# Kernel tuning notes

Hardware: AMD Instinct MI355X
Metric: run time of the kernel (lower is better)

Reference implementation:

```python
import jax, jax.numpy as jnp
import numpy as np

B, T, H = 16384, 64, 64
REG = 300
T10_LO, T10_HI = 0.2, 5.0
M0_LO, M0_HI = 0.1, 20.0


def setup_inputs() -> dict:
    key = jax.random.key(0)
    ks = jax.random.split(key, 40)
    std = 1.0 / np.sqrt(H)
    u = lambda k, shape: jax.random.uniform(k, shape, jnp.float32, -std, std)
    inp = {
        "X_fa": jax.random.normal(ks[0], (B, T), jnp.float32),
        "X_last": jax.random.normal(ks[1], (B, T), jnp.float32),
        "X_mean": jax.random.normal(ks[2], (B, T), jnp.float32),
        "X_mask": (jax.random.uniform(ks[3], (B, T)) < 0.7).astype(jnp.float32),
        "X_delta": jax.random.uniform(ks[4], (B, T), jnp.float32, 0.0, 2.0),
        "fa_vals": jax.random.uniform(ks[5], (B, T), jnp.float32, 0.05, 0.6),
        "TR_vals": jax.random.uniform(ks[6], (B, 1), jnp.float32, 0.003, 0.01),
        # GRU-D cell params (torch Linear convention: y = x @ W.T + b)
        "W_gx": u(ks[7], (1, 1)), "b_gx": u(ks[8], (1,)),
        "W_gh": u(ks[9], (H, 1)), "b_gh": u(ks[10], (H,)),
        "W_xc": u(ks[11], (3 * H, 1)), "b_xc": u(ks[12], (3 * H,)),
        "W_hn": u(ks[13], (H, H)),
        "W_hc": u(ks[14], (2 * H, H)),
        "W_mc": u(ks[15], (3 * H, 1)),
        # attention scores
        "W_sT": u(ks[16], (1, H)), "W_sM": u(ks[17], (1, H)),
        # reg_T10 MLP
        "Wt1": u(ks[18], (REG, H)), "bt1": u(ks[19], (REG,)),
        "Wt2": u(ks[20], (REG, REG)), "bt2": u(ks[21], (REG,)),
        "Wt3": u(ks[22], (1, REG)), "bt3": u(ks[23], (1,)),
        # reg_M0 MLP
        "Wm1": u(ks[24], (REG, H)), "bm1": u(ks[25], (REG,)),
        "Wm2": u(ks[26], (REG, REG)), "bm2": u(ks[27], (REG,)),
        "Wm3": u(ks[28], (1, REG)), "bm3": u(ks[29], (1,)),
    }
    return inp


def _forward(X_fa, X_last, X_mean, X_mask, X_delta, fa_vals, TR_vals,
             W_gx, b_gx, W_gh, b_gh, W_xc, b_xc, W_hn, W_hc, W_mc,
             W_sT, W_sM, Wt1, bt1, Wt2, bt2, Wt3, bt3, Wm1, bm1, Wm2, bm2, Wm3, bm3):
    Bv = X_fa.shape[0]
    Hd = W_gh.shape[0]
    tb = lambda a: a.T[:, :, None]  # [B,T] -> [T,B,1]
    xs = (tb(X_fa), tb(X_mask), tb(X_delta), tb(X_last), tb(X_mean))
    h0 = jnp.zeros((Bv, Hd), X_fa.dtype)

    def step(h, x):
        xi, m, d, xl, xm = x  # each [B,1]
        gx = jnp.exp(-jax.nn.relu(d @ W_gx.T + b_gx))            # [B,1]
        X = m * xi + (1 - m) * gx * xl + (1 - m) * (1 - gx) * xm  # [B,1]
        gh = jnp.exp(-jax.nn.relu(d @ W_gh.T + b_gh))            # [B,H]
        h = gh * h
        x_z, x_r, x_n = jnp.split(X @ W_xc.T + b_xc, 3, axis=1)
        h_z, h_r = jnp.split(h @ W_hc.T, 2, axis=1)
        m_z, m_r, m_n = jnp.split(m @ W_mc.T, 3, axis=1)
        z = jax.nn.sigmoid(x_z + h_z + m_z)
        r = jax.nn.sigmoid(x_r + h_r + m_r)
        h_til = jnp.tanh(x_n + (r * h) @ W_hn.T + m_n)
        h = (1 - z) * h + z * h_til
        return h, (h, X[:, 0])

    _, (out_tbh, Xg_tb) = jax.lax.scan(step, h0, xs)
    out = jnp.transpose(out_tbh, (1, 0, 2))  # [B,T,H]
    X_gru = Xg_tb.T                           # [B,T]

    sT = jax.nn.softmax(out @ W_sT.T, axis=1)  # [B,T,1], softmax over time
    sM = jax.nn.softmax(out @ W_sM.T, axis=1)
    hid_T = jnp.sum(out * sT, axis=1)  # [B,H]
    hid_M = jnp.sum(out * sM, axis=1)

    def reg(h, W1, b1, W2, b2, W3, b3):
        h = jax.nn.elu(h @ W1.T + b1)
        h = jax.nn.elu(h @ W2.T + b2)
        return h @ W3.T + b3  # [B,1]

    t_raw = reg(hid_T, Wt1, bt1, Wt2, bt2, Wt3, bt3)
    m_raw = reg(hid_M, Wm1, bm1, Wm2, bm2, Wm3, bm3)
    T10 = T10_LO + jax.nn.sigmoid(t_raw) * (T10_HI - T10_LO)  # [B,1]
    M0 = M0_LO + jax.nn.sigmoid(m_raw) * (M0_HI - M0_LO)      # [B,1]

    R1 = 1.0 / T10                       # [B,1]
    e = jnp.exp(-TR_vals * R1)           # [B,1]
    X_out = (1 - e) * jnp.sin(fa_vals) / (1 - jnp.cos(fa_vals) * e)  # [B,T]
    X_out = X_out * M0
    return X_out, T10, M0, out, X_gru


def reference(X_fa, X_last, X_mean, X_mask, X_delta, fa_vals, TR_vals,
              W_gx, b_gx, W_gh, b_gh, W_xc, b_xc, W_hn, W_hc, W_mc,
              W_sT, W_sM, Wt1, bt1, Wt2, bt2, Wt3, bt3, Wm1, bm1, Wm2, bm2, Wm3, bm3):
    return _forward(X_fa, X_last, X_mean, X_mask, X_delta, fa_vals, TR_vals,
                    W_gx, b_gx, W_gh, b_gh, W_xc, b_xc, W_hn, W_hc, W_mc,
                    W_sT, W_sM, Wt1, bt1, Wt2, bt2, Wt3, bt3, Wm1, bm1, Wm2, bm2, Wm3, bm3)
```

## Files before the change

### kernel.cpp

```cpp
#include <hip/hip_runtime.h>

#define B_N 16384
#define T_N 64
#define H_N 64
#define XOUT_OFF 0
#define T10_OFF  (B_N * T_N)
#define M0_OFF   (T10_OFF + B_N)
#define OUT_OFF  (M0_OFF + B_N)
#define XGRU_OFF (OUT_OFF + B_N * T_N * H_N)

#define WS_HIDT 0
#define WS_HIDM (WS_HIDT + B_N * 64 * 4)
#define WS_W1T_HI (WS_HIDM + B_N * 64 * 4)
#define WS_W1T_LO (WS_W1T_HI + 304 * 64 * 2)
#define WS_W1M_HI (WS_W1T_LO + 304 * 64 * 2)
#define WS_W1M_LO (WS_W1M_HI + 304 * 64 * 2)
#define WS_W2T_HI (WS_W1M_LO + 304 * 64 * 2)
#define WS_W2T_LO (WS_W2T_HI + 304 * 320 * 2)
#define WS_W2M_HI (WS_W2T_LO + 304 * 320 * 2)
#define WS_W2M_LO (WS_W2M_HI + 304 * 320 * 2)

typedef float  f32x4  __attribute__((ext_vector_type(4)));
typedef __bf16 bf16x8 __attribute__((ext_vector_type(8)));
typedef __bf16 bf16x4 __attribute__((ext_vector_type(4)));

__device__ __forceinline__ f32x4 mfma16(bf16x8 a, bf16x8 b, f32x4 c) {
  return __builtin_amdgcn_mfma_f32_16x16x32_bf16(a, b, c, 0, 0, 0);
}
__device__ __forceinline__ void split8v(const float* v, bf16x8& hi, bf16x8& lo) {
#pragma unroll
  for (int i = 0; i < 8; ++i) {
    __bf16 h = (__bf16)v[i];
    hi[i] = h;
    lo[i] = (__bf16)(v[i] - (float)h);
  }
}
__device__ __forceinline__ void split4v(const float* v, bf16x4& hi, bf16x4& lo) {
#pragma unroll
  for (int i = 0; i < 4; ++i) {
    __bf16 h = (__bf16)v[i];
    hi[i] = h;
    lo[i] = (__bf16)(v[i] - (float)h);
  }
}
__device__ __forceinline__ float sigm(float x) {
  return __builtin_amdgcn_rcpf(1.f + __expf(-x));
}
__device__ __forceinline__ float tanh_f(float x) {
  return 1.f - 2.f * __builtin_amdgcn_rcpf(__expf(2.f * x) + 1.f);
}

__global__ __launch_bounds__(256, 4) void k_gru(
    const float* __restrict__ Xfa, const float* __restrict__ Xlast,
    const float* __restrict__ Xmean, const float* __restrict__ Xmask,
    const float* __restrict__ Xdelta,
    const float* __restrict__ Wgx, const float* __restrict__ bgx,
    const float* __restrict__ Wgh, const float* __restrict__ bgh,
    const float* __restrict__ Wxc, const float* __restrict__ bxc,
    const float* __restrict__ Whn, const float* __restrict__ Whc,
    const float* __restrict__ Wmc,
    const float* __restrict__ WsT, const float* __restrict__ WsM,
    float* __restrict__ dout, float* __restrict__ hidT, float* __restrict__ hidM) {
  __shared__ __align__(16) unsigned char smem[33280];
  const int tid = threadIdx.x;
  const int wv = tid >> 6, l = tid & 63, b16 = l & 15, g4 = l >> 4;
  const int brow = blockIdx.x * 16 + b16;

  for (int c = tid; c < 1536; c += 256) {
    const float* src;
    int row, kc, base;
    if (c < 1024) { row = c >> 3; kc = c & 7; src = Whc + row * 64 + kc * 8; base = 0; }
    else { int c2 = c - 1024; row = c2 >> 3; kc = c2 & 7; src = Whn + row * 64 + kc * 8; base = 16384; }
    float v[8];
    *(float4*)&v[0] = *(const float4*)src;
    *(float4*)&v[4] = *(const float4*)(src + 4);
    bf16x8 hi, lo;
    split8v(v, hi, lo);
    *(bf16x8*)(smem + base + row * 128 + ((kc * 16) ^ ((row & 7) << 4))) = lo;
  }

  const int zrow = wv * 16 + b16;
  const int rrow = 64 + wv * 16 + b16;
  const int nrow = wv * 16 + b16;
  bf16x8 wz_hi[2], wr_hi[2], wn_hi[2];
#pragma unroll
  for (int kt = 0; kt < 2; ++kt) {
    float v[8];
    bf16x8 hi, lo;
    const float* s1 = Whc + zrow * 64 + kt * 32 + g4 * 8;
    *(float4*)&v[0] = *(const float4*)s1; *(float4*)&v[4] = *(const float4*)(s1 + 4);
    split8v(v, hi, lo); wz_hi[kt] = hi;
    const float* s2 = Whc + rrow * 64 + kt * 32 + g4 * 8;
    *(float4*)&v[0] = *(const float4*)s2; *(float4*)&v[4] = *(const float4*)(s2 + 4);
    split8v(v, hi, lo); wr_hi[kt] = hi;
    const float* s3 = Whn + nrow * 64 + kt * 32 + g4 * 8;
    *(float4*)&v[0] = *(const float4*)s3; *(float4*)&v[4] = *(const float4*)(s3 + 4);
    split8v(v, hi, lo); wn_hi[kt] = hi;
  }
  bf16x8 ez = {}, er = {}, en = {};
  if (g4 == 0) {
    const int jz = zrow, jr = rrow, jn = 128 + nrow;
    float Wv, Mv, bv;
    __bf16 wh, mh, bh;
#define MKEXT(dst, WIDX, MIDX, BIDX)                                   \
    Wv = Wxc[WIDX]; Mv = Wmc[MIDX]; bv = bxc[BIDX];                    \
    wh = (__bf16)Wv; mh = (__bf16)Mv; bh = (__bf16)bv;                 \
    dst[0] = wh; dst[1] = (__bf16)(Wv - (float)wh); dst[2] = wh;       \
    dst[3] = mh; dst[4] = (__bf16)(Mv - (float)mh);                    \
    dst[5] = bh; dst[6] = (__bf16)(bv - (float)bh); dst[7] = (__bf16)0.f;
    MKEXT(ez, jz, jz, jz)
    MKEXT(er, jr, jr, jr)
    MKEXT(en, jn, jn, jn)
#undef MKEXT
  }
  float wgh4[4], bgh4[4], wsT4[4], wsM4[4];
#pragma unroll
  for (int i = 0; i < 4; ++i) {
    const int j = wv * 16 + g4 * 4 + i;
    wgh4[i] = Wgh[j]; bgh4[i] = bgh[j];
    wsT4[i] = WsT[j]; wsM4[i] = WsM[j];
  }
  const float wgx0 = Wgx[0], bgx0 = bgx[0];

  __syncthreads();

  float hcur[4] = {}, aT[4] = {}, aM[4] = {};
  float lT = 0.f, lM = 0.f;

  const int ib = brow * T_N;
  float p_xi = Xfa[ib], p_mm = Xmask[ib], p_dd = Xdelta[ib], p_xl = Xlast[ib], p_xm = Xmean[ib];
  const int swz = (b16 & 7) << 4;
  float* outp = dout + OUT_OFF;

  for (int t = 0; t < T_N; ++t) {
    const float xi = p_xi, mm = p_mm, dd = p_dd, xl = p_xl, xm = p_xm;
    const int tn = (t + 1 < T_N) ? t + 1 : T_N - 1;
    p_xi = Xfa[ib + tn]; p_mm = Xmask[ib + tn]; p_dd = Xdelta[ib + tn];
    p_xl = Xlast[ib + tn]; p_xm = Xmean[ib + tn];

    float hd[4];
    {
      float v[4];
#pragma unroll
      for (int i = 0; i < 4; ++i) {
        const float gh = __expf(-fmaxf(0.f, dd * wgh4[i] + bgh4[i]));
        hd[i] = hcur[i] * gh;
        v[i] = hd[i];
      }
      bf16x4 hi4, lo4;
      split4v(v, hi4, lo4);
      const int off = (wv * 32 + g4 * 8) ^ swz;
      *(bf16x4*)(smem + 24576 + b16 * 128 + off) = hi4;
      *(bf16x4*)(smem + 26624 + b16 * 128 + off) = lo4;
    }
    const float gx = __expf(-fmaxf(0.f, dd * wgx0 + bgx0));
    const float X = mm * xi + (1.f - mm) * gx * xl + (1.f - mm) * (1.f - gx) * xm;
    if (wv == 0 && g4 == 0) dout[XGRU_OFF + ib + t] = X;
    bf16x8 bext = {};
    if (g4 == 0) {
      const __bf16 xh = (__bf16)X;
      bext[0] = xh; bext[1] = xh; bext[2] = (__bf16)(X - (float)xh);
      const __bf16 mb = (__bf16)mm;
      bext[3] = mb; bext[4] = mb;
      bext[5] = (__bf16)1.f; bext[6] = (__bf16)1.f; bext[7] = (__bf16)0.f;
    }
    __syncthreads();

    if (t > 0) {
      const f32x4 a = *(const f32x4*)(smem + 32768 + b16 * 32);
      const f32x4 c = *(const f32x4*)(smem + 32768 + b16 * 32 + 16);
      const float pT = __expf(a[0] + a[2] + c[0] + c[2]);
      const float pM = __expf(a[1] + a[3] + c[1] + c[3]);
      lT += pT; lM += pM;
#pragma unroll
      for (int i = 0; i < 4; ++i) { aT[i] += pT * hcur[i]; aM[i] += pM * hcur[i]; }
    }

    f32x4 accZ = {0.f, 0.f, 0.f, 0.f}, accR = {0.f, 0.f, 0.f, 0.f};
#pragma unroll
    for (int kt = 0; kt < 2; ++kt) {
      const int boff = (kt * 64 + g4 * 16) ^ swz;
      const bf16x8 bh = *(const bf16x8*)(smem + 24576 + b16 * 128 + boff);
      const bf16x8 bl = *(const bf16x8*)(smem + 26624 + b16 * 128 + boff);
      const int aoff = (kt * 64 + g4 * 16);
      const bf16x8 zlo = *(const bf16x8*)(smem + zrow * 128 + (aoff ^ ((zrow & 7) << 4)));
      const bf16x8 rlo = *(const bf16x8*)(smem + rrow * 128 + (aoff ^ ((rrow & 7) << 4)));
      accZ = mfma16(wz_hi[kt], bh, accZ);
      accZ = mfma16(zlo, bh, accZ);
      accZ = mfma16(wz_hi[kt], bl, accZ);
      accR = mfma16(wr_hi[kt], bh, accR);
      accR = mfma16(rlo, bh, accR);
      accR = mfma16(wr_hi[kt], bl, accR);
    }
    accZ = mfma16(ez, bext, accZ);
    accR = mfma16(er, bext, accR);

    float zz[4], rh[4];
#pragma unroll
    for (int i = 0; i < 4; ++i) {
      zz[i] = sigm(accZ[i]);
      rh[i] = sigm(accR[i]) * hd[i];
    }
    {
      bf16x4 hi4, lo4;
      split4v(rh, hi4, lo4);
      const int off = (wv * 32 + g4 * 8) ^ swz;
      *(bf16x4*)(smem + 28672 + b16 * 128 + off) = hi4;
      *(bf16x4*)(smem + 30720 + b16 * 128 + off) = lo4;
    }
    __syncthreads();

    f32x4 accN = {0.f, 0.f, 0.f, 0.f};
#pragma unroll
    for (int kt = 0; kt < 2; ++kt) {
      const int boff = (kt * 64 + g4 * 16) ^ swz;
      const bf16x8 ch = *(const bf16x8*)(smem + 28672 + b16 * 128 + boff);
      const bf16x8 cl = *(const bf16x8*)(smem + 30720 + b16 * 128 + boff);
      const bf16x8 nlo =
          *(const bf16x8*)(smem + 16384 + nrow * 128 + ((kt * 64 + g4 * 16) ^ ((nrow & 7) << 4)));
      accN = mfma16(wn_hi[kt], ch, accN);
      accN = mfma16(nlo, ch, accN);
      accN = mfma16(wn_hi[kt], cl, accN);
    }
    accN = mfma16(en, bext, accN);

    f32x4 ho;
    float scT = 0.f, scM = 0.f;
#pragma unroll
    for (int i = 0; i < 4; ++i) {
      const float ht = tanh_f(accN[i]);
      const float hn = (1.f - zz[i]) * hd[i] + zz[i] * ht;
      hcur[i] = hn;
      ho[i] = hn;
      scT += hn * wsT4[i];
      scM += hn * wsM4[i];
    }
    *(f32x4*)(outp + (ib + t) * 64 + wv * 16 + g4 * 4) = ho;
    scT += __shfl_xor(scT, 16); scT += __shfl_xor(scT, 32);
    scM += __shfl_xor(scM, 16); scM += __shfl_xor(scM, 32);
    if (l < 16) {
      float2 sc = {scT, scM};
      *(float2*)(smem + 32768 + b16 * 32 + wv * 8) = sc;
    }
  }
  __syncthreads();
  {
    const f32x4 a = *(const f32x4*)(smem + 32768 + b16 * 32);
    const f32x4 c = *(const f32x4*)(smem + 32768 + b16 * 32 + 16);
    const float pT = __expf(a[0] + a[2] + c[0] + c[2]);
    const float pM = __expf(a[1] + a[3] + c[1] + c[3]);
    lT += pT; lM += pM;
#pragma unroll
    for (int i = 0; i < 4; ++i) { aT[i] += pT * hcur[i]; aM[i] += pM * hcur[i]; }
  }
  const float invT = 1.f / lT, invM = 1.f / lM;
  f32x4 vT, vM;
#pragma unroll
  for (int i = 0; i < 4; ++i) { vT[i] = aT[i] * invT; vM[i] = aM[i] * invM; }
  *(f32x4*)(hidT + brow * 64 + wv * 16 + g4 * 4) = vT;
  *(f32x4*)(hidM + brow * 64 + wv * 16 + g4 * 4) = vM;
}

__device__ __forceinline__ void wsplit(float v, unsigned short* hi, unsigned short* lo, int idx) {
  union { __bf16 b; unsigned short u; } c;
  __bf16 hb = (__bf16)v;
  c.b = hb; hi[idx] = c.u;
  c.b = (__bf16)(v - (float)hb); lo[idx] = c.u;
}
__global__ void k_prep(const float* __restrict__ Wt1, const float* __restrict__ Wm1,
                       const float* __restrict__ Wt2, const float* __restrict__ Wm2,
                       unsigned short* w1t_hi, unsigned short* w1t_lo,
                       unsigned short* w1m_hi, unsigned short* w1m_lo,
                       unsigned short* w2t_hi, unsigned short* w2t_lo,
                       unsigned short* w2m_hi, unsigned short* w2m_lo) {
  const int i = blockIdx.x * 256 + threadIdx.x;
  if (i < 304 * 64) {
    const int r = i >> 6, c = i & 63;
    const float vt = (r < 300) ? Wt1[r * 64 + c] : 0.f;
    const float vm = (r < 300) ? Wm1[r * 64 + c] : 0.f;
    wsplit(vt, w1t_hi, w1t_lo, i);
    wsplit(vm, w1m_hi, w1m_lo, i);
  }
  {
    const int r = i / 320, c = i - r * 320;
    const bool ok = (r < 300) && (c < 300);
    const float vt = ok ? Wt2[r * 300 + c] : 0.f;
    const float vm = ok ? Wm2[r * 300 + c] : 0.f;
    wsplit(vt, w2t_hi, w2t_lo, i);
    wsplit(vm, w2m_hi, w2m_lo, i);
  }
}

__global__ __launch_bounds__(256, 2) void k_mlp(
    const float* __restrict__ hidT, const float* __restrict__ hidM,
    const unsigned short* __restrict__ w1t_hi, const unsigned short* __restrict__ w1t_lo,
    const unsigned short* __restrict__ w1m_hi, const unsigned short* __restrict__ w1m_lo,
    const unsigned short* __restrict__ w2t_hi, const unsigned short* __restrict__ w2t_lo,
    const unsigned short* __restrict__ w2m_hi, const unsigned short* __restrict__ w2m_lo,
    const float* __restrict__ bt1, const float* __restrict__ bt2,
    const float* __restrict__ Wt3, const float* __restrict__ bt3,
    const float* __restrict__ bm1, const float* __restrict__ bm2,
    const float* __restrict__ Wm3, const float* __restrict__ bm3,
    float* __restrict__ dout) {
  __shared__ __align__(16) unsigned char smem[44608];
  const int tid = threadIdx.x;
  const int blk = blockIdx.x & 255;
  const bool isM = blockIdx.x >= 256;
  const float* hid = isM ? hidM : hidT;
  const unsigned short* w1hi = isM ? w1m_hi : w1t_hi;
  const unsigned short* w1lo = isM ? w1m_lo : w1t_lo;
  const unsigned short* w2hi = isM ? w2m_hi : w2t_hi;
  const unsigned short* w2lo = isM ? w2m_lo : w2t_lo;
  const float* b1 = isM ? bm1 : bt1;
  const float* b2 = isM ? bm2 : bt2;
  const float* w3 = isM ? Wm3 : Wt3;
  const float b3 = (isM ? bm3 : bt3)[0];
  const float LOV = isM ? 0.1f : 0.2f;
  const float HIV = isM ? 20.f : 5.0f;
  float* headp = dout + (isM ? M0_OFF : T10_OFF);

  float* sb1 = (float*)(smem + 40960);
  float* sb2 = (float*)(smem + 42176);
  float* sw3 = (float*)(smem + 43392);
  for (int i = tid; i < 304; i += 256) {
    sb1[i] = (i < 300) ? b1[i] : 0.f;
    sb2[i] = (i < 300) ? b2[i] : 0.f;
    sw3[i] = (i < 300) ? w3[i] : 0.f;
  }
  __syncthreads();

  const int wv = tid >> 6, l = tid & 63, b16 = l & 15, g4 = l >> 4;
  const int b = blk * 64 + wv * 16 + b16;
  const int h1off = wv * 10240;

  bf16x8 b1h[2], b1l[2];
#pragma unroll
  for (int kt = 0; kt < 2; ++kt) {
    const float* hp = hid + b * 64 + kt * 32 + g4 * 8;
    float v[8];
    *(float4*)&v[0] = *(const float4*)hp;
    *(float4*)&v[4] = *(const float4*)(hp + 4);
    split8v(v, b1h[kt], b1l[kt]);
  }
  f32x4 acc1[19];
#pragma unroll
  for (int jt = 0; jt < 19; ++jt) {
    f32x4 acc = {0.f, 0.f, 0.f, 0.f};
#pragma unroll
    for (int kt = 0; kt < 2; ++kt) {
      const int row = jt * 16 + b16;
      bf16x8 ahi = *(const bf16x8*)(w1hi + row * 64 + kt * 32 + g4 * 8);
      bf16x8 alo = *(const bf16x8*)(w1lo + row * 64 + kt * 32 + g4 * 8);
      acc = mfma16(ahi, b1h[kt], acc);
      acc = mfma16(alo, b1h[kt], acc);
      acc = mfma16(ahi, b1l[kt], acc);
    }
    acc1[jt] = acc;
  }
  if (g4 == 0) {
#pragma unroll
    for (int q = 0; q < 4; ++q) {
      const int off = (608 + q * 8) ^ ((b16 & 7) << 4);
      *(unsigned long long*)(smem + h1off + b16 * 640 + off) = 0ull;
    }
  }
#pragma unroll
  for (int jt = 0; jt < 19; ++jt) {
    bf16x4 hv;
#pragma unroll
    for (int i = 0; i < 4; ++i) {
      const int j = jt * 16 + g4 * 4 + i;
      const float v = acc1[jt][i] + sb1[j];
      const float e = (v > 0.f) ? v : (__expf(v) - 1.f);
      hv[i] = (__bf16)e;
    }
    const int off = (jt * 32 + g4 * 8) ^ ((b16 & 7) << 4);
    *(bf16x4*)(smem + h1off + b16 * 640 + off) = hv;
  }
  bf16x8 bh2[10];
#pragma unroll
  for (int kt = 0; kt < 10; ++kt) {
    const int off = (kt * 64 + g4 * 16) ^ ((b16 & 7) << 4);
    bh2[kt] = *(const bf16x8*)(smem + h1off + b16 * 640 + off);
  }
  float raw = 0.f;
#pragma unroll
  for (int jt = 0; jt < 19; ++jt) {
    f32x4 acc = {0.f, 0.f, 0.f, 0.f};
#pragma unroll
    for (int kt = 0; kt < 10; ++kt) {
      const int row = jt * 16 + b16;
      bf16x8 ahi = *(const bf16x8*)(w2hi + row * 320 + kt * 32 + g4 * 8);
      bf16x8 alo = *(const bf16x8*)(w2lo + row * 320 + kt * 32 + g4 * 8);
      acc = mfma16(ahi, bh2[kt], acc);
      acc = mfma16(alo, bh2[kt], acc);
    }
#pragma unroll
    for (int i = 0; i < 4; ++i) {
      const int j = jt * 16 + g4 * 4 + i;
      const float v = acc[i] + sb2[j];
      const float e = (v > 0.f) ? v : (__expf(v) - 1.f);
      raw += e * sw3[j];
    }
  }
  raw += __shfl_xor(raw, 16);
  raw += __shfl_xor(raw, 32);
  if (l < 16) {
    const float rr = raw + b3;
    headp[b] = LOV + (HIV - LOV) / (1.f + __expf(-rr));
  }
}

__global__ void k_final(const float* __restrict__ fav, const float* __restrict__ TR,
                        float* __restrict__ dout) {
  const int i = blockIdx.x * 256 + threadIdx.x;
  const int bb = i >> 6;
  const float T10v = dout[T10_OFF + bb];
  const float M0v = dout[M0_OFF + bb];
  const float e = __expf(-TR[bb] / T10v);
  const float fa = fav[i];
  float s, c;
  __sincosf(fa, &s, &c);
  dout[i] = (1.f - e) * s / (1.f - c * e) * M0v;
}

extern "C" void kernel_launch(void* const* d_in, const int* in_sizes, int n_in,
                              void* d_out, int out_size, void* d_ws, size_t ws_size,
                              hipStream_t stream) {
  const float* Xfa   = (const float*)d_in[0];
  const float* Xlast = (const float*)d_in[1];
  const float* Xmean = (const float*)d_in[2];
  const float* Xmask = (const float*)d_in[3];
  const float* Xdelta= (const float*)d_in[4];
  const float* fav   = (const float*)d_in[5];
  const float* TR    = (const float*)d_in[6];
  const float* Wgx   = (const float*)d_in[7];
  const float* bgx   = (const float*)d_in[8];
  const float* Wgh   = (const float*)d_in[9];
  const float* bgh   = (const float*)d_in[10];
  const float* Wxc   = (const float*)d_in[11];
  const float* bxc   = (const float*)d_in[12];
  const float* Whn   = (const float*)d_in[13];
  const float* Whc   = (const float*)d_in[14];
  const float* Wmc   = (const float*)d_in[15];
  const float* WsT   = (const float*)d_in[16];
  const float* WsM   = (const float*)d_in[17];
  const float* Wt1   = (const float*)d_in[18];
  const float* bt1   = (const float*)d_in[19];
  const float* Wt2   = (const float*)d_in[20];
  const float* bt2   = (const float*)d_in[21];
  const float* Wt3   = (const float*)d_in[22];
  const float* bt3   = (const float*)d_in[23];
  const float* Wm1   = (const float*)d_in[24];
  const float* bm1   = (const float*)d_in[25];
  const float* Wm2   = (const float*)d_in[26];
  const float* bm2   = (const float*)d_in[27];
  const float* Wm3   = (const float*)d_in[28];
  const float* bm3   = (const float*)d_in[29];

  float* dout = (float*)d_out;
  char* ws = (char*)d_ws;
  float* hidT = (float*)(ws + WS_HIDT);
  float* hidM = (float*)(ws + WS_HIDM);
  unsigned short* w1t_hi = (unsigned short*)(ws + WS_W1T_HI);
  unsigned short* w1t_lo = (unsigned short*)(ws + WS_W1T_LO);
  unsigned short* w1m_hi = (unsigned short*)(ws + WS_W1M_HI);
  unsigned short* w1m_lo = (unsigned short*)(ws + WS_W1M_LO);
  unsigned short* w2t_hi = (unsigned short*)(ws + WS_W2T_HI);
  unsigned short* w2t_lo = (unsigned short*)(ws + WS_W2T_LO);
  unsigned short* w2m_hi = (unsigned short*)(ws + WS_W2M_HI);
  unsigned short* w2m_lo = (unsigned short*)(ws + WS_W2M_LO);

  k_prep<<<380, 256, 0, stream>>>(Wt1, Wm1, Wt2, Wm2, w1t_hi, w1t_lo, w1m_hi, w1m_lo,
                                  w2t_hi, w2t_lo, w2m_hi, w2m_lo);
  k_gru<<<1024, 256, 0, stream>>>(Xfa, Xlast, Xmean, Xmask, Xdelta, Wgx, bgx, Wgh, bgh, Wxc, bxc,
                                  Whn, Whc, Wmc, WsT, WsM, dout, hidT, hidM);
  k_mlp<<<512, 256, 0, stream>>>(hidT, hidM, w1t_hi, w1t_lo, w1m_hi, w1m_lo, w2t_hi, w2t_lo,
                                 w2m_hi, w2m_lo, bt1, bt2, Wt3, bt3, bm1, bm2, Wm3, bm3, dout);
  k_final<<<4096, 256, 0, stream>>>(fav, TR, dout);
}
```

Before: 697.0 us.

## Stage GRU outputs in LDS for coalesced stores, keep Whn lo in registers

```diff
diff --git a/kernel.cpp b/kernel.cpp
--- a/kernel.cpp
+++ b/kernel.cpp
@@ -49,6 +49,20 @@
 __device__ __forceinline__ float tanh_f(float x) {
   return 1.f - 2.f * __builtin_amdgcn_rcpf(__expf(2.f * x) + 1.f);
 }
+__device__ __forceinline__ void wave_barrier() {
+  asm volatile("s_waitcnt lgkmcnt(0)" ::: "memory");
+  __builtin_amdgcn_s_barrier();
+  __builtin_amdgcn_sched_barrier(0);
+}
+
+#define OS_WHCLO 0
+#define OS_HDH 16384
+#define OS_HDL 18432
+#define OS_RHH 20480
+#define OS_RHL 22528
+#define OS_SC  24576
+#define OS_OST 25088
+#define OS_XST 29440
 
 __global__ __launch_bounds__(256, 4) void k_gru(
     const float* __restrict__ Xfa, const float* __restrict__ Xlast,
@@ -61,28 +75,26 @@
     const float* __restrict__ Wmc,
     const float* __restrict__ WsT, const float* __restrict__ WsM,
     float* __restrict__ dout, float* __restrict__ hidT, float* __restrict__ hidM) {
-  __shared__ __align__(16) unsigned char smem[33280];
+  __shared__ __align__(16) unsigned char smem[33792];
   const int tid = threadIdx.x;
   const int wv = tid >> 6, l = tid & 63, b16 = l & 15, g4 = l >> 4;
   const int brow = blockIdx.x * 16 + b16;
 
-  for (int c = tid; c < 1536; c += 256) {
-    const float* src;
-    int row, kc, base;
-    if (c < 1024) { row = c >> 3; kc = c & 7; src = Whc + row * 64 + kc * 8; base = 0; }
-    else { int c2 = c - 1024; row = c2 >> 3; kc = c2 & 7; src = Whn + row * 64 + kc * 8; base = 16384; }
+  for (int c = tid; c < 1024; c += 256) {
+    const int row = c >> 3, kc = c & 7;
+    const float* src = Whc + row * 64 + kc * 8;
     float v[8];
     *(float4*)&v[0] = *(const float4*)src;
     *(float4*)&v[4] = *(const float4*)(src + 4);
     bf16x8 hi, lo;
     split8v(v, hi, lo);
-    *(bf16x8*)(smem + base + row * 128 + ((kc * 16) ^ ((row & 7) << 4))) = lo;
+    *(bf16x8*)(smem + OS_WHCLO + row * 128 + ((kc * 16) ^ ((row & 7) << 4))) = lo;
   }
 
   const int zrow = wv * 16 + b16;
   const int rrow = 64 + wv * 16 + b16;
   const int nrow = wv * 16 + b16;
-  bf16x8 wz_hi[2], wr_hi[2], wn_hi[2];
+  bf16x8 wz_hi[2], wr_hi[2], wn_hi[2], wn_lo[2];
 #pragma unroll
   for (int kt = 0; kt < 2; ++kt) {
     float v[8];
@@ -95,7 +107,7 @@
     split8v(v, hi, lo); wr_hi[kt] = hi;
     const float* s3 = Whn + nrow * 64 + kt * 32 + g4 * 8;
     *(float4*)&v[0] = *(const float4*)s3; *(float4*)&v[4] = *(const float4*)(s3 + 4);
-    split8v(v, hi, lo); wn_hi[kt] = hi;
+    split8v(v, hi, lo); wn_hi[kt] = hi; wn_lo[kt] = lo;
   }
   bf16x8 ez = {}, er = {}, en = {};
   if (g4 == 0) {
@@ -131,6 +143,9 @@
   float p_xi = Xfa[ib], p_mm = Xmask[ib], p_dd = Xdelta[ib], p_xl = Xlast[ib], p_xm = Xmean[ib];
   const int swz = (b16 & 7) << 4;
   float* outp = dout + OUT_OFF;
+  const int orow = wv * 4 + (l >> 4);
+  const int ocol = (l & 15) * 4;
+  const long obase = (long)(blockIdx.x * 16 + orow) * 64;
 
   for (int t = 0; t < T_N; ++t) {
     const float xi = p_xi, mm = p_mm, dd = p_dd, xl = p_xl, xm = p_xm;
@@ -150,12 +165,12 @@
       bf16x4 hi4, lo4;
       split4v(v, hi4, lo4);
       const int off = (wv * 32 + g4 * 8) ^ swz;
-      *(bf16x4*)(smem + 24576 + b16 * 128 + off) = hi4;
-      *(bf16x4*)(smem + 26624 + b16 * 128 + off) = lo4;
+      *(bf16x4*)(smem + OS_HDH + b16 * 128 + off) = hi4;
+      *(bf16x4*)(smem + OS_HDL + b16 * 128 + off) = lo4;
     }
     const float gx = __expf(-fmaxf(0.f, dd * wgx0 + bgx0));
     const float X = mm * xi + (1.f - mm) * gx * xl + (1.f - mm) * (1.f - gx) * xm;
-    if (wv == 0 && g4 == 0) dout[XGRU_OFF + ib + t] = X;
+    if (wv == 0 && g4 == 0) *(float*)(smem + OS_XST + b16 * 272 + t * 4) = X;
     bf16x8 bext = {};
     if (g4 == 0) {
       const __bf16 xh = (__bf16)X;
@@ -164,11 +179,15 @@
       bext[3] = mb; bext[4] = mb;
       bext[5] = (__bf16)1.f; bext[6] = (__bf16)1.f; bext[7] = (__bf16)0.f;
     }
-    __syncthreads();
+    wave_barrier();
 
     if (t > 0) {
-      const f32x4 a = *(const f32x4*)(smem + 32768 + b16 * 32);
-      const f32x4 c = *(const f32x4*)(smem + 32768 + b16 * 32 + 16);
+      const f32x4 hv = *(const f32x4*)(smem + OS_OST + orow * 272 + ocol * 4);
+      *(f32x4*)(outp + (obase + (t - 1)) * 64 + ocol) = hv;
+    }
+    if (t > 0) {
+      const f32x4 a = *(const f32x4*)(smem + OS_SC + b16 * 32);
+      const f32x4 c = *(const f32x4*)(smem + OS_SC + b16 * 32 + 16);
       const float pT = __expf(a[0] + a[2] + c[0] + c[2]);
       const float pM = __expf(a[1] + a[3] + c[1] + c[3]);
       lT += pT; lM += pM;
@@ -176,77 +195,89 @@
       for (int i = 0; i < 4; ++i) { aT[i] += pT * hcur[i]; aM[i] += pM * hcur[i]; }
     }
 
-    f32x4 accZ = {0.f, 0.f, 0.f, 0.f}, accR = {0.f, 0.f, 0.f, 0.f};
+    f32x4 za = {0.f, 0.f, 0.f, 0.f}, zb = za, ra = za, rb = za;
+    bf16x8 bh[2], bl[2];
 #pragma unroll
     for (int kt = 0; kt < 2; ++kt) {
       const int boff = (kt * 64 + g4 * 16) ^ swz;
-      const bf16x8 bh = *(const bf16x8*)(smem + 24576 + b16 * 128 + boff);
-      const bf16x8 bl = *(const bf16x8*)(smem + 26624 + b16 * 128 + boff);
-      const int aoff = (kt * 64 + g4 * 16);
-      const bf16x8 zlo = *(const bf16x8*)(smem + zrow * 128 + (aoff ^ ((zrow & 7) << 4)));
-      const bf16x8 rlo = *(const bf16x8*)(smem + rrow * 128 + (aoff ^ ((rrow & 7) << 4)));
-      accZ = mfma16(wz_hi[kt], bh, accZ);
-      accZ = mfma16(zlo, bh, accZ);
-      accZ = mfma16(wz_hi[kt], bl, accZ);
-      accR = mfma16(wr_hi[kt], bh, accR);
-      accR = mfma16(rlo, bh, accR);
-      accR = mfma16(wr_hi[kt], bl, accR);
-    }
-    accZ = mfma16(ez, bext, accZ);
-    accR = mfma16(er, bext, accR);
+      bh[kt] = *(const bf16x8*)(smem + OS_HDH + b16 * 128 + boff);
+      bl[kt] = *(const bf16x8*)(smem + OS_HDL + b16 * 128 + boff);
+    }
+#pragma unroll
+    for (int kt = 0; kt < 2; ++kt) {
+      const int aoff = kt * 64 + g4 * 16;
+      const bf16x8 zlo = *(const bf16x8*)(smem + OS_WHCLO + zrow * 128 + (aoff ^ ((zrow & 7) << 4)));
+      const bf16x8 rlo = *(const bf16x8*)(smem + OS_WHCLO + rrow * 128 + (aoff ^ ((rrow & 7) << 4)));
+      za = mfma16(wz_hi[kt], bh[kt], za);
+      zb = mfma16(zlo, bh[kt], zb);
+      ra = mfma16(wr_hi[kt], bh[kt], ra);
+      rb = mfma16(rlo, bh[kt], rb);
+    }
+#pragma unroll
+    for (int kt = 0; kt < 2; ++kt) {
+      zb = mfma16(wz_hi[kt], bl[kt], zb);
+      rb = mfma16(wr_hi[kt], bl[kt], rb);
+    }
+    za = mfma16(ez, bext, za);
+    ra = mfma16(er, bext, ra);
 
     float zz[4], rh[4];
 #pragma unroll
     for (int i = 0; i < 4; ++i) {
-      zz[i] = sigm(accZ[i]);
-      rh[i] = sigm(accR[i]) * hd[i];
+      zz[i] = sigm(za[i] + zb[i]);
+      rh[i] = sigm(ra[i] + rb[i]) * hd[i];
     }
     {
       bf16x4 hi4, lo4;
       split4v(rh, hi4, lo4);
       const int off = (wv * 32 + g4 * 8) ^ swz;
-      *(bf16x4*)(smem + 28672 + b16 * 128 + off) = hi4;
-      *(bf16x4*)(smem + 30720 + b16 * 128 + off) = lo4;
-    }
-    __syncthreads();
-
-    f32x4 accN = {0.f, 0.f, 0.f, 0.f};
+      *(bf16x4*)(smem + OS_RHH + b16 * 128 + off) = hi4;
+      *(bf16x4*)(smem + OS_RHL + b16 * 128 + off) = lo4;
+    }
+    wave_barrier();
+
+    f32x4 na = {0.f, 0.f, 0.f, 0.f}, nb = na;
 #pragma unroll
     for (int kt = 0; kt < 2; ++kt) {
       const int boff = (kt * 64 + g4 * 16) ^ swz;
-      const bf16x8 ch = *(const bf16x8*)(smem + 28672 + b16 * 128 + boff);
-      const bf16x8 cl = *(const bf16x8*)(smem + 30720 + b16 * 128 + boff);
-      const bf16x8 nlo =
-          *(const bf16x8*)(smem + 16384 + nrow * 128 + ((kt * 64 + g4 * 16) ^ ((nrow & 7) << 4)));
-      accN = mfma16(wn_hi[kt], ch, accN);
-      accN = mfma16(nlo, ch, accN);
-      accN = mfma16(wn_hi[kt], cl, accN);
-    }
-    accN = mfma16(en, bext, accN);
-
+      const bf16x8 ch = *(const bf16x8*)(smem + OS_RHH + b16 * 128 + boff);
+      const bf16x8 cl = *(const bf16x8*)(smem + OS_RHL + b16 * 128 + boff);
+      na = mfma16(wn_hi[kt], ch, na);
+      nb = mfma16(wn_lo[kt], ch, nb);
+      nb = mfma16(wn_hi[kt], cl, nb);
+    }
+    na = mfma16(en, bext, na);
+
+    float scT = 0.f, scM = 0.f;
     f32x4 ho;
-    float scT = 0.f, scM = 0.f;
 #pragma unroll
     for (int i = 0; i < 4; ++i) {
-      const float ht = tanh_f(accN[i]);
+      const float ht = tanh_f(na[i] + nb[i]);
       const float hn = (1.f - zz[i]) * hd[i] + zz[i] * ht;
       hcur[i] = hn;
       ho[i] = hn;
       scT += hn * wsT4[i];
       scM += hn * wsM4[i];
     }
-    *(f32x4*)(outp + (ib + t) * 64 + wv * 16 + g4 * 4) = ho;
+    *(f32x4*)(smem + OS_OST + b16 * 272 + (wv * 16 + g4 * 4) * 4) = ho;
     scT += __shfl_xor(scT, 16); scT += __shfl_xor(scT, 32);
     scM += __shfl_xor(scM, 16); scM += __shfl_xor(scM, 32);
     if (l < 16) {
       float2 sc = {scT, scM};
-      *(float2*)(smem + 32768 + b16 * 32 + wv * 8) = sc;
-    }
-  }
-  __syncthreads();
+      *(float2*)(smem + OS_SC + b16 * 32 + wv * 8) = sc;
+    }
+  }
+  wave_barrier();
+
   {
-    const f32x4 a = *(const f32x4*)(smem + 32768 + b16 * 32);
-    const f32x4 c = *(const f32x4*)(smem + 32768 + b16 * 32 + 16);
+    const f32x4 hv = *(const f32x4*)(smem + OS_OST + orow * 272 + ocol * 4);
+    *(f32x4*)(outp + (obase + 63) * 64 + ocol) = hv;
+    const f32x4 xv = *(const f32x4*)(smem + OS_XST + orow * 272 + ocol * 4);
+    *(f32x4*)(dout + XGRU_OFF + obase + ocol) = xv;
+  }
+  {
+    const f32x4 a = *(const f32x4*)(smem + OS_SC + b16 * 32);
+    const f32x4 c = *(const f32x4*)(smem + OS_SC + b16 * 32 + 16);
     const float pT = __expf(a[0] + a[2] + c[0] + c[2]);
     const float pM = __expf(a[1] + a[3] + c[1] + c[3]);
     lT += pT; lM += pM;
```

Result: slower. 817.1 us (+17.2%).
